# Optimization experiments

Measured on AMD Instinct MI355X. Metric: run time of the kernel, lower is better.

## Reference

```python
import jax, jax.numpy as jnp
import numpy as np

R = 256   # resolution
C = 16    # n_chan
F = 8     # n_freq
N = 262144


def setup_inputs() -> dict:
    key = jax.random.key(0)
    k1, k2 = jax.random.split(key)
    coords = jax.random.uniform(k1, (N, 3), dtype=jnp.float32, minval=-1.0, maxval=1.0)
    grid = jax.random.normal(k2, (3, C * F, R, R), dtype=jnp.float32) * 0.1
    # matches torch init: linspace(0,1,C*F).reshape(-1,C).T.reshape(-1)
    freqs = jnp.linspace(0.0, 1.0, C * F, dtype=jnp.float32).reshape(-1, C).T.reshape(-1)
    return {"coords": coords, "grid": grid, "freqs": freqs}


def _reflect(x, size):
    # PyTorch grid_sample reflection padding, align_corners=True:
    # reflect unnormalized coords about [0, size-1], period 2*(size-1)
    span = size - 1
    m = 2 * span
    r = jnp.abs(x) % m
    return jnp.where(r > span, m - r, r)


def _grid_sample_plane(img, xy):
    # img: (CF, R, R); xy: (Npts, 2) normalized [-1,1], (x indexes W, y indexes H)
    ix = _reflect((xy[:, 0] + 1.0) * 0.5 * (R - 1), R)
    iy = _reflect((xy[:, 1] + 1.0) * 0.5 * (R - 1), R)
    x0f = jnp.floor(ix); y0f = jnp.floor(iy)
    wx = ix - x0f; wy = iy - y0f
    x0 = jnp.clip(x0f.astype(jnp.int32), 0, R - 1)
    x1 = jnp.clip(x0 + 1, 0, R - 1)
    y0 = jnp.clip(y0f.astype(jnp.int32), 0, R - 1)
    y1 = jnp.clip(y0 + 1, 0, R - 1)
    v00 = img[:, y0, x0]  # (CF, Npts)
    v01 = img[:, y0, x1]
    v10 = img[:, y1, x0]
    v11 = img[:, y1, x1]
    return (v00 * (1 - wx) * (1 - wy) + v01 * wx * (1 - wy)
            + v10 * (1 - wx) * wy + v11 * wx * wy)


def reference(coords, grid, freqs):
    n = coords.shape[0]
    # tri-plane sample coords: plane0 (y,z), plane1 (x,z), plane2 (x,y)
    xy = jnp.stack([coords[:, (1, 2)], coords[:, (0, 2)], coords[:, (0, 1)]], 0)  # (3,N,2)
    coefs = jax.vmap(_grid_sample_plane)(grid, xy)          # (3, CF, N)
    coefs = coefs.transpose(2, 1, 0).reshape(n, C, F, 3)    # (N, C, F, 3)
    # get_freqs(): 2**(clamp(freqs,0,1)*log2(R)) - 1
    fr = 2.0 ** (jnp.clip(freqs, 0.0, 1.0) * np.float32(np.log2(R))) - 1.0  # (CF,)
    pts = (coords + 1.0) * 0.5 * (R - 1)                    # (N, 3)
    phase = (jnp.pi / R) * (pts[:, None, None, :] + 0.5) * (fr.reshape(C, F)[None, :, :, None] + 0.5)
    basis = jnp.cos(phase)                                   # (N, C, F, 3)
    # einsum BCFT,BCFT->BCT then sum over T == sum over (F, T)
    return 2.0 * jnp.sum(coefs * basis, axis=(2, 3))         # (N, C)
```

## Files before the change

### kernel.cpp

```cpp
#include <hip/hip_runtime.h>

#define RES   256
#define NCH   128
#define NC    16
#define QG    32
#define NPK   64
#define NBINS 4096
#define TBLK  3072

__device__ __forceinline__ unsigned int f32_to_bf16_rne(float f) {
    unsigned int u = __float_as_uint(f);
    return (u + 0x7FFFu + ((u >> 16) & 1u)) >> 16;
}
__device__ __forceinline__ float bf16_lo(unsigned int w) {
    return __uint_as_float(w << 16);
}
__device__ __forceinline__ float bf16_hi(unsigned int w) {
    return __uint_as_float(w & 0xFFFF0000u);
}
__device__ __forceinline__ float reflectf(float v) {
    float r = fabsf(v);
    r = fmodf(r, 510.0f);
    return (r > 255.0f) ? (510.0f - r) : r;
}
__device__ __forceinline__ unsigned spread3(unsigned v) {
    return (v & 1u) | ((v & 2u) << 2) | ((v & 4u) << 4) | ((v & 8u) << 6);
}
__device__ __forceinline__ int point_cell(const float* __restrict__ coords, int i) {
    const float r0 = reflectf((coords[3 * (size_t)i + 0] + 1.0f) * 127.5f);
    const float r1 = reflectf((coords[3 * (size_t)i + 1] + 1.0f) * 127.5f);
    const float r2 = reflectf((coords[3 * (size_t)i + 2] + 1.0f) * 127.5f);
    const unsigned cx = (unsigned)min(max((int)r0, 0), 255) >> 4;
    const unsigned cy = (unsigned)min(max((int)r1, 0), 255) >> 4;
    const unsigned cz = (unsigned)min(max((int)r2, 0), 255) >> 4;
    return (int)(spread3(cx) | (spread3(cy) << 1) | (spread3(cz) << 2));
}

__global__ __launch_bounds__(256) void fg_transpose_hist(
    const float* __restrict__ in, unsigned int* __restrict__ out,
    const float* __restrict__ coords, unsigned* __restrict__ hist, int n)
{
    __shared__ float tile[QG][RES + 4];
    const int tid = threadIdx.x;
    const int qg = blockIdx.x;
    const int y  = blockIdx.y;
    const int p  = blockIdx.z;

    {
        const int bid = (p * RES + y) * 4 + qg;
        const int per = (n + TBLK - 1) / TBLK;
        const int s0 = bid * per;
        const int s1 = min(s0 + per, n);
        for (int k = s0 + tid; k < s1; k += 256)
            atomicAdd(&hist[point_cell(coords, k)], 1u);
    }

    const int q0 = qg * QG;
    const float* src = in + (((size_t)p * NCH + q0) * RES + y) * RES;
    #pragma unroll
    for (int it = 0; it < (QG * RES / 4) / 256; ++it) {
        const int lin = it * 256 + tid;
        const int qq = lin >> 6;
        const int x4 = lin & 63;
        *(float4*)&tile[qq][x4 * 4] =
            *(const float4*)(src + (size_t)qq * (RES * RES) + x4 * 4);
    }
    __syncthreads();
    unsigned int* dst = out + (((size_t)p * RES + y) * RES) * NPK + (q0 >> 1);
    #pragma unroll
    for (int it = 0; it < (RES * (QG / 2)) / 256; ++it) {
        const int lin = it * 256 + tid;
        const int qp = lin & 15;
        const int x  = lin >> 4;
        const unsigned int lo = f32_to_bf16_rne(tile[2 * qp + 0][x]);
        const unsigned int hi = f32_to_bf16_rne(tile[2 * qp + 1][x]);
        dst[(size_t)x * NPK + qp] = lo | (hi << 16);
    }
}

__global__ __launch_bounds__(256) void fg_scan(
    const unsigned* __restrict__ hist, unsigned* __restrict__ cursor,
    const float* __restrict__ freqs, float* __restrict__ frp)
{
    __shared__ unsigned wtot[4];
    const int t = threadIdx.x;
    const int lane = t & 63;
    const int wid = t >> 6;
    unsigned loc[16];
    unsigned sum = 0;
    #pragma unroll
    for (int k = 0; k < 16; ++k) { loc[k] = hist[t * 16 + k]; sum += loc[k]; }
    unsigned v = sum;
    #pragma unroll
    for (int off = 1; off < 64; off <<= 1) {
        unsigned u = __shfl_up(v, off);
        if (lane >= off) v += u;
    }
    if (lane == 63) wtot[wid] = v;
    __syncthreads();
    unsigned base = 0;
    #pragma unroll
    for (int w = 0; w < 4; ++w) base += (w < wid) ? wtot[w] : 0u;
    unsigned run = base + (v - sum);
    #pragma unroll
    for (int k = 0; k < 16; ++k) { cursor[t * 16 + k] = run; run += loc[k]; }
    if (t < 128) {
        const float f = fminf(fmaxf(freqs[t], 0.0f), 1.0f);
        frp[t] = __builtin_amdgcn_exp2f(f * 8.0f) - 0.5f;
    }
}

__global__ __launch_bounds__(256) void fg_scatter(
    const float* __restrict__ coords, unsigned* __restrict__ cursor,
    unsigned* __restrict__ perm, int n)
{
    const int i = blockIdx.x * 256 + threadIdx.x;
    if (i >= n) return;
    const unsigned pos = atomicAdd(&cursor[point_cell(coords, i)], 1u);
    perm[pos] = (unsigned)i;
}

__global__ __launch_bounds__(256) void fg_main_bf16(
    const float* __restrict__ coords,
    const unsigned int* __restrict__ grid,
    const float* __restrict__ frp_in,
    const unsigned* __restrict__ perm,
    float* __restrict__ out, int n)
{
    const int t = threadIdx.x;
    const int c = t & 15;
    int b = blockIdx.x;
    {
        const int G = gridDim.x;
        const int chunk = G >> 3;
        const int lim = chunk << 3;
        if (b < lim) b = (b & 7) * chunk + (b >> 3);
    }
    const int slot = b * 16 + (t >> 4);
    if (slot >= n) return;
    const int i = (int)perm[slot];

    float frp[8];
    *(float4*)(frp + 0) = *(const float4*)(frp_in + c * 8 + 0);
    *(float4*)(frp + 4) = *(const float4*)(frp_in + c * 8 + 4);

    const float c0 = coords[3 * (size_t)i + 0];
    const float c1 = coords[3 * (size_t)i + 1];
    const float c2 = coords[3 * (size_t)i + 2];
    const float pts0 = (c0 + 1.0f) * 127.5f;
    const float pts1 = (c1 + 1.0f) * 127.5f;
    const float pts2 = (c2 + 1.0f) * 127.5f;

    float acc = 0.0f;

    #pragma unroll
    for (int p = 0; p < 3; ++p) {
        const float sx = (p == 0) ? pts1 : pts0;
        const float sy = (p == 2) ? pts1 : pts2;
        const float pp = (p == 0) ? pts0 : ((p == 1) ? pts1 : pts2);

        const float ix = reflectf(sx);
        const float iy = reflectf(sy);
        const float x0f = floorf(ix), y0f = floorf(iy);
        const float wx = ix - x0f, wy = iy - y0f;
        int x0 = (int)x0f; x0 = min(max(x0, 0), RES - 1);
        int y0 = (int)y0f; y0 = min(max(y0, 0), RES - 1);
        const int x1 = min(x0 + 1, RES - 1);
        const int y1 = min(y0 + 1, RES - 1);
        const float w00 = (1.0f - wx) * (1.0f - wy);
        const float w01 = wx * (1.0f - wy);
        const float w10 = (1.0f - wx) * wy;
        const float w11 = wx * wy;
        const float A = (pp + 0.5f) * (1.0f / 512.0f);

        const size_t rowbase = ((size_t)p * RES) * RES;
        const unsigned int* b00 = grid + (rowbase + (size_t)y0 * RES + x0) * NPK + c * 4;
        const unsigned int* b01 = grid + (rowbase + (size_t)y0 * RES + x1) * NPK + c * 4;
        const unsigned int* b10 = grid + (rowbase + (size_t)y1 * RES + x0) * NPK + c * 4;
        const unsigned int* b11 = grid + (rowbase + (size_t)y1 * RES + x1) * NPK + c * 4;
        const uint4 g00 = *(const uint4*)b00;
        const uint4 g01 = *(const uint4*)b01;
        const uint4 g10 = *(const uint4*)b10;
        const uint4 g11 = *(const uint4*)b11;
        const unsigned int w0[4] = {g00.x, g00.y, g00.z, g00.w};
        const unsigned int w1[4] = {g01.x, g01.y, g01.z, g01.w};
        const unsigned int w2[4] = {g10.x, g10.y, g10.z, g10.w};
        const unsigned int w3[4] = {g11.x, g11.y, g11.z, g11.w};

        #pragma unroll
        for (int jj = 0; jj < 4; ++jj) {
            const float clo = w00 * bf16_lo(w0[jj]) + w01 * bf16_lo(w1[jj])
                            + w10 * bf16_lo(w2[jj]) + w11 * bf16_lo(w3[jj]);
            const float chi = w00 * bf16_hi(w0[jj]) + w01 * bf16_hi(w1[jj])
                            + w10 * bf16_hi(w2[jj]) + w11 * bf16_hi(w3[jj]);
            const float rl = __builtin_amdgcn_fractf(A * frp[2 * jj + 0]);
            const float rh = __builtin_amdgcn_fractf(A * frp[2 * jj + 1]);
            acc += clo * __builtin_amdgcn_cosf(rl);
            acc += chi * __builtin_amdgcn_cosf(rh);
        }
    }

    out[(size_t)i * NC + c] = 2.0f * acc;
}

__global__ __launch_bounds__(256) void fg_main_f32(
    const float* __restrict__ coords,
    const float* __restrict__ grid,
    const float* __restrict__ freqs,
    float* __restrict__ out, int n)
{
    const int t = threadIdx.x;
    const int c = t & 15;
    const int i = blockIdx.x * 16 + (t >> 4);
    if (i >= n) return;

    float frp[8];
    #pragma unroll
    for (int j = 0; j < 8; ++j) {
        float f = fminf(fmaxf(freqs[c * 8 + j], 0.0f), 1.0f);
        frp[j] = __builtin_amdgcn_exp2f(f * 8.0f) - 0.5f;
    }
    const float c0 = coords[3 * (size_t)i + 0];
    const float c1 = coords[3 * (size_t)i + 1];
    const float c2 = coords[3 * (size_t)i + 2];
    const float pts0 = (c0 + 1.0f) * 127.5f;
    const float pts1 = (c1 + 1.0f) * 127.5f;
    const float pts2 = (c2 + 1.0f) * 127.5f;
    float acc = 0.0f;
    #pragma unroll
    for (int p = 0; p < 3; ++p) {
        const float sx = (p == 0) ? pts1 : pts0;
        const float sy = (p == 2) ? pts1 : pts2;
        const float pp = (p == 0) ? pts0 : ((p == 1) ? pts1 : pts2);
        const float ix = reflectf(sx);
        const float iy = reflectf(sy);
        const float x0f = floorf(ix), y0f = floorf(iy);
        const float wx = ix - x0f, wy = iy - y0f;
        int x0 = (int)x0f; x0 = min(max(x0, 0), RES - 1);
        int y0 = (int)y0f; y0 = min(max(y0, 0), RES - 1);
        const int x1 = min(x0 + 1, RES - 1);
        const int y1 = min(y0 + 1, RES - 1);
        const float w00 = (1.0f - wx) * (1.0f - wy);
        const float w01 = wx * (1.0f - wy);
        const float w10 = (1.0f - wx) * wy;
        const float w11 = wx * wy;
        const float A = (pp + 0.5f) * (1.0f / 512.0f);
        const size_t plane = (size_t)p * NCH * RES * RES;
        const int o00 = y0 * RES + x0, o01 = y0 * RES + x1;
        const int o10 = y1 * RES + x0, o11 = y1 * RES + x1;
        #pragma unroll
        for (int j = 0; j < 8; ++j) {
            const float* gq = grid + plane + (size_t)(c * 8 + j) * (RES * RES);
            const float coef = w00 * gq[o00] + w01 * gq[o01]
                             + w10 * gq[o10] + w11 * gq[o11];
            const float rr = __builtin_amdgcn_fractf(A * frp[j]);
            acc += coef * __builtin_amdgcn_cosf(rr);
        }
    }
    out[(size_t)i * NC + c] = 2.0f * acc;
}

extern "C" void kernel_launch(void* const* d_in, const int* in_sizes, int n_in,
                              void* d_out, int out_size, void* d_ws, size_t ws_size,
                              hipStream_t stream)
{
    const float* coords = (const float*)d_in[0];
    const float* grid   = (const float*)d_in[1];
    const float* freqs  = (const float*)d_in[2];
    float* out = (float*)d_out;
    const int n = in_sizes[0] / 3;

    const size_t gridT_b  = (size_t)3 * RES * RES * NPK * sizeof(unsigned);
    const size_t hist_b   = (size_t)NBINS * sizeof(unsigned);
    const size_t frp_b    = 128 * sizeof(float);
    const size_t perm_b   = (size_t)((n + 3) & ~3) * sizeof(unsigned);
    const size_t need = gridT_b + 2 * hist_b + frp_b + perm_b;

    const int blocks = (n + 15) / 16;

    if (ws_size >= need) {
        char* ws = (char*)d_ws;
        unsigned* gridT  = (unsigned*)ws;                 ws += gridT_b;
        unsigned* hist   = (unsigned*)ws;                 ws += hist_b;
        unsigned* cursor = (unsigned*)ws;                 ws += hist_b;
        float*    frp    = (float*)ws;                    ws += frp_b;
        unsigned* perm   = (unsigned*)ws;

        hipMemsetAsync(hist, 0, hist_b, stream);
        hipLaunchKernelGGL(fg_transpose_hist, dim3(4, RES, 3), dim3(256), 0, stream,
                           grid, gridT, coords, hist, n);
        hipLaunchKernelGGL(fg_scan, dim3(1), dim3(256), 0, stream,
                           hist, cursor, freqs, frp);
        hipLaunchKernelGGL(fg_scatter, dim3((n + 255) / 256), dim3(256), 0, stream,
                           coords, cursor, perm, n);
        hipLaunchKernelGGL(fg_main_bf16, dim3(blocks), dim3(256), 0, stream,
                           coords, gridT, frp, perm, out, n);
    } else {
        hipLaunchKernelGGL(fg_main_f32, dim3(blocks), dim3(256), 0, stream,
                           coords, grid, freqs, out, n);
    }
}
```

Baseline: 244.3 us.

## Precompute sorted per-point sample records and use finer spatial bins

The scatter pass now writes a 48-byte record per point in sorted order. Each record holds the precomputed byte offsets into the transposed grid for all three planes, the interpolation fractions, the phase factors and the original index, so the main kernel no longer gathers coords through the permutation or redoes the reflect and floor math. Morton binning moves from 16-voxel to 8-voxel cells (32768 bins), with a 1024-thread scan, to tighten gather locality. The histogram is split out of the transpose, and the transpose becomes a non-LDS kernel where each thread packs 8 channels into a uint4 store. In exchange it writes and reads much more intermediate data per point, and the unclamped +1 neighbor offset relies on a zero weight at the edge.

Measured after the change: 273.6 us. 1.12x slower.

```diff
diff --git a/kernel.cpp b/kernel.cpp
--- a/kernel.cpp
+++ b/kernel.cpp
@@ -3,107 +3,101 @@
 #define RES   256
 #define NCH   128
 #define NC    16
-#define QG    32
 #define NPK   64
-#define NBINS 4096
-#define TBLK  3072
-
-__device__ __forceinline__ unsigned int f32_to_bf16_rne(float f) {
-    unsigned int u = __float_as_uint(f);
+#define NBINS 32768
+#define RECW  12
+
+__device__ __forceinline__ unsigned f32_to_bf16_rne(float f) {
+    unsigned u = __float_as_uint(f);
     return (u + 0x7FFFu + ((u >> 16) & 1u)) >> 16;
 }
-__device__ __forceinline__ float bf16_lo(unsigned int w) {
-    return __uint_as_float(w << 16);
-}
-__device__ __forceinline__ float bf16_hi(unsigned int w) {
-    return __uint_as_float(w & 0xFFFF0000u);
-}
+__device__ __forceinline__ float bf16_lo(unsigned w) { return __uint_as_float(w << 16); }
+__device__ __forceinline__ float bf16_hi(unsigned w) { return __uint_as_float(w & 0xFFFF0000u); }
 __device__ __forceinline__ float reflectf(float v) {
     float r = fabsf(v);
     r = fmodf(r, 510.0f);
     return (r > 255.0f) ? (510.0f - r) : r;
 }
-__device__ __forceinline__ unsigned spread3(unsigned v) {
-    return (v & 1u) | ((v & 2u) << 2) | ((v & 4u) << 4) | ((v & 8u) << 6);
+__device__ __forceinline__ unsigned spread5(unsigned v) {
+    return (v & 1u) | ((v & 2u) << 2) | ((v & 4u) << 4) | ((v & 8u) << 6) | ((v & 16u) << 8);
+}
+__device__ __forceinline__ int cell_of(int x0, int x1, int x2) {
+    return (int)(spread5((unsigned)x0 >> 3) | (spread5((unsigned)x1 >> 3) << 1)
+               | (spread5((unsigned)x2 >> 3) << 2));
 }
 __device__ __forceinline__ int point_cell(const float* __restrict__ coords, int i) {
-    const float r0 = reflectf((coords[3 * (size_t)i + 0] + 1.0f) * 127.5f);
-    const float r1 = reflectf((coords[3 * (size_t)i + 1] + 1.0f) * 127.5f);
-    const float r2 = reflectf((coords[3 * (size_t)i + 2] + 1.0f) * 127.5f);
-    const unsigned cx = (unsigned)min(max((int)r0, 0), 255) >> 4;
-    const unsigned cy = (unsigned)min(max((int)r1, 0), 255) >> 4;
-    const unsigned cz = (unsigned)min(max((int)r2, 0), 255) >> 4;
-    return (int)(spread3(cx) | (spread3(cy) << 1) | (spread3(cz) << 2));
-}
-
-__global__ __launch_bounds__(256) void fg_transpose_hist(
-    const float* __restrict__ in, unsigned int* __restrict__ out,
+    const int a = (int)reflectf((coords[3 * (size_t)i + 0] + 1.0f) * 127.5f);
+    const int b = (int)reflectf((coords[3 * (size_t)i + 1] + 1.0f) * 127.5f);
+    const int d = (int)reflectf((coords[3 * (size_t)i + 2] + 1.0f) * 127.5f);
+    return cell_of(a, b, d);
+}
+
+__global__ __launch_bounds__(256) void fg_transpose(
+    const float* __restrict__ in, unsigned* __restrict__ out)
+{
+    const int tid = threadIdx.x;
+    const int x   = blockIdx.x * 128 + (tid & 127);
+    const int g0  = (tid >> 7) * 8;
+    const int y   = blockIdx.y;
+    const int p   = blockIdx.z;
+
+    const float* src = in + (((size_t)p * NCH) * RES + y) * RES + x;
+    unsigned* dst = out + (((size_t)p * RES + y) * RES + x) * NPK;
+
+    #pragma unroll
+    for (int g = g0; g < g0 + 8; ++g) {
+        float v[8];
+        #pragma unroll
+        for (int j = 0; j < 8; ++j)
+            v[j] = src[(size_t)(g * 8 + j) * (RES * RES)];
+        uint4 w;
+        w.x = f32_to_bf16_rne(v[0]) | (f32_to_bf16_rne(v[1]) << 16);
+        w.y = f32_to_bf16_rne(v[2]) | (f32_to_bf16_rne(v[3]) << 16);
+        w.z = f32_to_bf16_rne(v[4]) | (f32_to_bf16_rne(v[5]) << 16);
+        w.w = f32_to_bf16_rne(v[6]) | (f32_to_bf16_rne(v[7]) << 16);
+        *(uint4*)(dst + 4 * g) = w;
+    }
+}
+
+__global__ __launch_bounds__(256) void fg_hist(
     const float* __restrict__ coords, unsigned* __restrict__ hist, int n)
 {
-    __shared__ float tile[QG][RES + 4];
-    const int tid = threadIdx.x;
-    const int qg = blockIdx.x;
-    const int y  = blockIdx.y;
-    const int p  = blockIdx.z;
-
-    {
-        const int bid = (p * RES + y) * 4 + qg;
-        const int per = (n + TBLK - 1) / TBLK;
-        const int s0 = bid * per;
-        const int s1 = min(s0 + per, n);
-        for (int k = s0 + tid; k < s1; k += 256)
-            atomicAdd(&hist[point_cell(coords, k)], 1u);
-    }
-
-    const int q0 = qg * QG;
-    const float* src = in + (((size_t)p * NCH + q0) * RES + y) * RES;
-    #pragma unroll
-    for (int it = 0; it < (QG * RES / 4) / 256; ++it) {
-        const int lin = it * 256 + tid;
-        const int qq = lin >> 6;
-        const int x4 = lin & 63;
-        *(float4*)&tile[qq][x4 * 4] =
-            *(const float4*)(src + (size_t)qq * (RES * RES) + x4 * 4);
-    }
-    __syncthreads();
-    unsigned int* dst = out + (((size_t)p * RES + y) * RES) * NPK + (q0 >> 1);
-    #pragma unroll
-    for (int it = 0; it < (RES * (QG / 2)) / 256; ++it) {
-        const int lin = it * 256 + tid;
-        const int qp = lin & 15;
-        const int x  = lin >> 4;
-        const unsigned int lo = f32_to_bf16_rne(tile[2 * qp + 0][x]);
-        const unsigned int hi = f32_to_bf16_rne(tile[2 * qp + 1][x]);
-        dst[(size_t)x * NPK + qp] = lo | (hi << 16);
-    }
-}
-
-__global__ __launch_bounds__(256) void fg_scan(
+    const int i = blockIdx.x * 256 + threadIdx.x;
+    if (i >= n) return;
+    atomicAdd(&hist[point_cell(coords, i)], 1u);
+}
+
+__global__ __launch_bounds__(1024) void fg_scan(
     const unsigned* __restrict__ hist, unsigned* __restrict__ cursor,
     const float* __restrict__ freqs, float* __restrict__ frp)
 {
-    __shared__ unsigned wtot[4];
+    __shared__ unsigned wtot[16];
     const int t = threadIdx.x;
     const int lane = t & 63;
     const int wid = t >> 6;
-    unsigned loc[16];
+    unsigned loc[32];
     unsigned sum = 0;
     #pragma unroll
-    for (int k = 0; k < 16; ++k) { loc[k] = hist[t * 16 + k]; sum += loc[k]; }
+    for (int k = 0; k < 8; ++k) {
+        const uint4 u = ((const uint4*)hist)[t * 8 + k];
+        loc[4 * k + 0] = u.x; loc[4 * k + 1] = u.y;
+        loc[4 * k + 2] = u.z; loc[4 * k + 3] = u.w;
+        sum += u.x + u.y + u.z + u.w;
+    }
     unsigned v = sum;
     #pragma unroll
     for (int off = 1; off < 64; off <<= 1) {
-        unsigned u = __shfl_up(v, off);
+        const unsigned u = __shfl_up(v, off);
         if (lane >= off) v += u;
     }
     if (lane == 63) wtot[wid] = v;
     __syncthreads();
     unsigned base = 0;
     #pragma unroll
-    for (int w = 0; w < 4; ++w) base += (w < wid) ? wtot[w] : 0u;
+    for (int w = 0; w < 16; ++w) base += (w < wid) ? wtot[w] : 0u;
     unsigned run = base + (v - sum);
     #pragma unroll
-    for (int k = 0; k < 16; ++k) { cursor[t * 16 + k] = run; run += loc[k]; }
+    for (int k = 0; k < 32; ++k) { cursor[t * 32 + k] = run; run += loc[k]; }
     if (t < 128) {
         const float f = fminf(fmaxf(freqs[t], 0.0f), 1.0f);
         frp[t] = __builtin_amdgcn_exp2f(f * 8.0f) - 0.5f;
@@ -112,19 +106,44 @@
 
 __global__ __launch_bounds__(256) void fg_scatter(
     const float* __restrict__ coords, unsigned* __restrict__ cursor,
-    unsigned* __restrict__ perm, int n)
+    unsigned* __restrict__ rec, int n)
 {
     const int i = blockIdx.x * 256 + threadIdx.x;
     if (i >= n) return;
-    const unsigned pos = atomicAdd(&cursor[point_cell(coords, i)], 1u);
-    perm[pos] = (unsigned)i;
+    int   x0[3];
+    float w[3], A[3];
+    #pragma unroll
+    for (int k = 0; k < 3; ++k) {
+        const float pts = (coords[3 * (size_t)i + k] + 1.0f) * 127.5f;
+        const float r = reflectf(pts);
+        const float fl = floorf(r);
+        x0[k] = (int)fl;
+        w[k]  = r - fl;
+        A[k]  = (pts + 0.5f) * (1.0f / 512.0f);
+    }
+    const unsigned pos = atomicAdd(&cursor[cell_of(x0[0], x0[1], x0[2])], 1u);
+    unsigned* o = rec + (size_t)pos * RECW;
+    uint4 r0, r1, r2;
+    r0.x = (unsigned)((x0[2] * 256 + x0[1]) * 256);
+    r0.y = (unsigned)((65536 + x0[2] * 256 + x0[0]) * 256);
+    r0.z = (unsigned)((131072 + x0[1] * 256 + x0[0]) * 256);
+    r0.w = __float_as_uint(w[0]);
+    r1.x = __float_as_uint(w[1]);
+    r1.y = __float_as_uint(w[2]);
+    r1.z = __float_as_uint(A[0]);
+    r1.w = __float_as_uint(A[1]);
+    r2.x = __float_as_uint(A[2]);
+    r2.y = (unsigned)i;
+    r2.z = 0u; r2.w = 0u;
+    *(uint4*)(o + 0) = r0;
+    *(uint4*)(o + 4) = r1;
+    *(uint4*)(o + 8) = r2;
 }
 
 __global__ __launch_bounds__(256) void fg_main_bf16(
-    const float* __restrict__ coords,
-    const unsigned int* __restrict__ grid,
+    const unsigned* __restrict__ grid,
     const float* __restrict__ frp_in,
-    const unsigned* __restrict__ perm,
+    const unsigned* __restrict__ rec,
     float* __restrict__ out, int n)
 {
     const int t = threadIdx.x;
@@ -138,63 +157,53 @@
     }
     const int slot = b * 16 + (t >> 4);
     if (slot >= n) return;
-    const int i = (int)perm[slot];
+
+    const unsigned* o = rec + (size_t)slot * RECW;
+    const uint4 r0 = *(const uint4*)(o + 0);
+    const uint4 r1 = *(const uint4*)(o + 4);
+    const uint4 r2 = *(const uint4*)(o + 8);
+    const unsigned off[3] = {r0.x, r0.y, r0.z};
+    const float w0 = __uint_as_float(r0.w);
+    const float w1 = __uint_as_float(r1.x);
+    const float w2 = __uint_as_float(r1.y);
+    const float A[3] = {__uint_as_float(r1.z), __uint_as_float(r1.w),
+                        __uint_as_float(r2.x)};
+    const int i = (int)r2.y;
 
     float frp[8];
     *(float4*)(frp + 0) = *(const float4*)(frp_in + c * 8 + 0);
     *(float4*)(frp + 4) = *(const float4*)(frp_in + c * 8 + 4);
 
-    const float c0 = coords[3 * (size_t)i + 0];
-    const float c1 = coords[3 * (size_t)i + 1];
-    const float c2 = coords[3 * (size_t)i + 2];
-    const float pts0 = (c0 + 1.0f) * 127.5f;
-    const float pts1 = (c1 + 1.0f) * 127.5f;
-    const float pts2 = (c2 + 1.0f) * 127.5f;
-
+    const char* gB = (const char*)grid;
+    const unsigned claneoff = (unsigned)(c * 16);
     float acc = 0.0f;
 
     #pragma unroll
     for (int p = 0; p < 3; ++p) {
-        const float sx = (p == 0) ? pts1 : pts0;
-        const float sy = (p == 2) ? pts1 : pts2;
-        const float pp = (p == 0) ? pts0 : ((p == 1) ? pts1 : pts2);
-
-        const float ix = reflectf(sx);
-        const float iy = reflectf(sy);
-        const float x0f = floorf(ix), y0f = floorf(iy);
-        const float wx = ix - x0f, wy = iy - y0f;
-        int x0 = (int)x0f; x0 = min(max(x0, 0), RES - 1);
-        int y0 = (int)y0f; y0 = min(max(y0, 0), RES - 1);
-        const int x1 = min(x0 + 1, RES - 1);
-        const int y1 = min(y0 + 1, RES - 1);
-        const float w00 = (1.0f - wx) * (1.0f - wy);
-        const float w01 = wx * (1.0f - wy);
-        const float w10 = (1.0f - wx) * wy;
-        const float w11 = wx * wy;
-        const float A = (pp + 0.5f) * (1.0f / 512.0f);
-
-        const size_t rowbase = ((size_t)p * RES) * RES;
-        const unsigned int* b00 = grid + (rowbase + (size_t)y0 * RES + x0) * NPK + c * 4;
-        const unsigned int* b01 = grid + (rowbase + (size_t)y0 * RES + x1) * NPK + c * 4;
-        const unsigned int* b10 = grid + (rowbase + (size_t)y1 * RES + x0) * NPK + c * 4;
-        const unsigned int* b11 = grid + (rowbase + (size_t)y1 * RES + x1) * NPK + c * 4;
-        const uint4 g00 = *(const uint4*)b00;
-        const uint4 g01 = *(const uint4*)b01;
-        const uint4 g10 = *(const uint4*)b10;
-        const uint4 g11 = *(const uint4*)b11;
-        const unsigned int w0[4] = {g00.x, g00.y, g00.z, g00.w};
-        const unsigned int w1[4] = {g01.x, g01.y, g01.z, g01.w};
-        const unsigned int w2[4] = {g10.x, g10.y, g10.z, g10.w};
-        const unsigned int w3[4] = {g11.x, g11.y, g11.z, g11.w};
+        const float wx = (p == 0) ? w1 : w0;
+        const float wy = (p == 2) ? w1 : w2;
+        const float ox = 1.0f - wx, oy = 1.0f - wy;
+        const float w00 = ox * oy, w01 = wx * oy, w10 = ox * wy, w11 = wx * wy;
+
+        const unsigned v0 = off[p] + claneoff;
+        const unsigned v1 = v0 + 65536u;
+        const uint4 g00 = *(const uint4*)(gB + v0);
+        const uint4 g01 = *(const uint4*)(gB + v0 + 256);
+        const uint4 g10 = *(const uint4*)(gB + v1);
+        const uint4 g11 = *(const uint4*)(gB + v1 + 256);
+        const unsigned a0[4] = {g00.x, g00.y, g00.z, g00.w};
+        const unsigned a1[4] = {g01.x, g01.y, g01.z, g01.w};
+        const unsigned a2[4] = {g10.x, g10.y, g10.z, g10.w};
+        const unsigned a3[4] = {g11.x, g11.y, g11.z, g11.w};
 
         #pragma unroll
         for (int jj = 0; jj < 4; ++jj) {
-            const float clo = w00 * bf16_lo(w0[jj]) + w01 * bf16_lo(w1[jj])
-                            + w10 * bf16_lo(w2[jj]) + w11 * bf16_lo(w3[jj]);
-            const float chi = w00 * bf16_hi(w0[jj]) + w01 * bf16_hi(w1[jj])
-                            + w10 * bf16_hi(w2[jj]) + w11 * bf16_hi(w3[jj]);
-            const float rl = __builtin_amdgcn_fractf(A * frp[2 * jj + 0]);
-            const float rh = __builtin_amdgcn_fractf(A * frp[2 * jj + 1]);
+            const float clo = w00 * bf16_lo(a0[jj]) + w01 * bf16_lo(a1[jj])
+                            + w10 * bf16_lo(a2[jj]) + w11 * bf16_lo(a3[jj]);
+            const float chi = w00 * bf16_hi(a0[jj]) + w01 * bf16_hi(a1[jj])
+                            + w10 * bf16_hi(a2[jj]) + w11 * bf16_hi(a3[jj]);
+            const float rl = __builtin_amdgcn_fractf(A[p] * frp[2 * jj + 0]);
+            const float rh = __builtin_amdgcn_fractf(A[p] * frp[2 * jj + 1]);
             acc += clo * __builtin_amdgcn_cosf(rl);
             acc += chi * __builtin_amdgcn_cosf(rh);
         }
@@ -244,7 +253,7 @@
         const float w01 = wx * (1.0f - wy);
         const float w10 = (1.0f - wx) * wy;
         const float w11 = wx * wy;
-        const float A = (pp + 0.5f) * (1.0f / 512.0f);
+        const float Ap = (pp + 0.5f) * (1.0f / 512.0f);
         const size_t plane = (size_t)p * NCH * RES * RES;
         const int o00 = y0 * RES + x0, o01 = y0 * RES + x1;
         const int o10 = y1 * RES + x0, o11 = y1 * RES + x1;
@@ -253,7 +262,7 @@
             const float* gq = grid + plane + (size_t)(c * 8 + j) * (RES * RES);
             const float coef = w00 * gq[o00] + w01 * gq[o01]
                              + w10 * gq[o10] + w11 * gq[o11];
-            const float rr = __builtin_amdgcn_fractf(A * frp[j]);
+            const float rr = __builtin_amdgcn_fractf(Ap * frp[j]);
             acc += coef * __builtin_amdgcn_cosf(rr);
         }
     }
@@ -270,31 +279,33 @@
     float* out = (float*)d_out;
     const int n = in_sizes[0] / 3;
 
-    const size_t gridT_b  = (size_t)3 * RES * RES * NPK * sizeof(unsigned);
-    const size_t hist_b   = (size_t)NBINS * sizeof(unsigned);
-    const size_t frp_b    = 128 * sizeof(float);
-    const size_t perm_b   = (size_t)((n + 3) & ~3) * sizeof(unsigned);
-    const size_t need = gridT_b + 2 * hist_b + frp_b + perm_b;
+    const size_t gridT_b = (size_t)3 * RES * RES * NPK * sizeof(unsigned);
+    const size_t hist_b  = (size_t)NBINS * sizeof(unsigned);
+    const size_t frp_b   = 128 * sizeof(float);
+    const size_t rec_b   = (size_t)n * RECW * sizeof(unsigned);
+    const size_t need = gridT_b + 2 * hist_b + frp_b + rec_b;
 
     const int blocks = (n + 15) / 16;
 
     if (ws_size >= need) {
         char* ws = (char*)d_ws;
-        unsigned* gridT  = (unsigned*)ws;                 ws += gridT_b;
-        unsigned* hist   = (unsigned*)ws;                 ws += hist_b;
-        unsigned* cursor = (unsigned*)ws;                 ws += hist_b;
-        float*    frp    = (float*)ws;                    ws += frp_b;
-        unsigned* perm   = (unsigned*)ws;
+        unsigned* gridT  = (unsigned*)ws;  ws += gridT_b;
+        unsigned* hist   = (unsigned*)ws;  ws += hist_b;
+        unsigned* cursor = (unsigned*)ws;  ws += hist_b;
+        float*    frp    = (float*)ws;     ws += frp_b;
+        unsigned* rec    = (unsigned*)ws;
 
         hipMemsetAsync(hist, 0, hist_b, stream);
-        hipLaunchKernelGGL(fg_transpose_hist, dim3(4, RES, 3), dim3(256), 0, stream,
-                           grid, gridT, coords, hist, n);
-        hipLaunchKernelGGL(fg_scan, dim3(1), dim3(256), 0, stream,
+        hipLaunchKernelGGL(fg_hist, dim3((n + 255) / 256), dim3(256), 0, stream,
+                           coords, hist, n);
+        hipLaunchKernelGGL(fg_transpose, dim3(2, RES, 3), dim3(256), 0, stream,
+                           grid, gridT);
+        hipLaunchKernelGGL(fg_scan, dim3(1), dim3(1024), 0, stream,
                            hist, cursor, freqs, frp);
         hipLaunchKernelGGL(fg_scatter, dim3((n + 255) / 256), dim3(256), 0, stream,
-                           coords, cursor, perm, n);
+                           coords, cursor, rec, n);
         hipLaunchKernelGGL(fg_main_bf16, dim3(blocks), dim3(256), 0, stream,
-                           coords, gridT, frp, perm, out, n);
+                           gridT, frp, rec, out, n);
     } else {
         hipLaunchKernelGGL(fg_main_f32, dim3(blocks), dim3(256), 0, stream,
                            coords, grid, freqs, out, n);
```
